# Performance work log

Hardware: AMD Instinct MI355X
Metric: run time of the kernel (lower is better)

The kernel has to match this reference:

```python
import jax, jax.numpy as jnp
import numpy as np

N_NODES = 50000
N_EDGES = 800000
IN_C, HID_C, OUT_C = 128, 128, 64


def setup_inputs() -> dict:
    key = jax.random.key(0)
    k1, k2, k3, k4 = jax.random.split(key, 4)
    x = jax.random.normal(k1, (N_NODES, IN_C), dtype=jnp.float32)
    edge_index = jax.random.randint(k2, (2, N_EDGES), 0, N_NODES, dtype=jnp.int64)
    # Glorot-ish init for weights, zero bias (PyG GCNConv default has bias)
    W1 = jax.random.normal(k3, (IN_C, HID_C), dtype=jnp.float32) * (1.0 / np.sqrt(IN_C))
    b1 = jnp.zeros((HID_C,), dtype=jnp.float32)
    W2 = jax.random.normal(k4, (HID_C, OUT_C), dtype=jnp.float32) * (1.0 / np.sqrt(HID_C))
    b2 = jnp.zeros((OUT_C,), dtype=jnp.float32)
    return {"x": x, "edge_index": edge_index, "W1": W1, "b1": b1, "W2": W2, "b2": b2}


def _gcn_norm(edge_index, num_nodes):
    """PyG gcn_norm: add self-loops, symmetric deg^{-1/2} normalization."""
    loop = jnp.arange(num_nodes, dtype=edge_index.dtype)
    src = jnp.concatenate([edge_index[0], loop])  # [E + N]
    dst = jnp.concatenate([edge_index[1], loop])
    ones = jnp.ones(src.shape[0], dtype=jnp.float32)
    deg = jax.ops.segment_sum(ones, dst, num_segments=num_nodes)  # in-degree incl. self-loop
    dinv = jnp.where(deg > 0, jax.lax.rsqrt(deg), 0.0)
    norm = dinv[src] * dinv[dst]  # [E + N]
    return src, dst, norm


def _gcn_conv(x, W, b, src, dst, norm, num_nodes):
    h = x @ W                                   # [N, C_out] transform first (PyG order)
    msg = h[src] * norm[:, None]                # gather + normalize, [E+N, C_out]
    out = jax.ops.segment_sum(msg, dst, num_segments=num_nodes)  # scatter-add
    return out + b


def reference(x, edge_index, W1, b1, W2, b2):
    N = x.shape[0]
    src, dst, norm = _gcn_norm(edge_index, N)  # graph normalization shared by both layers
    h = jax.nn.relu(_gcn_conv(x, W1, b1, src, dst, norm, N))
    out = _gcn_conv(h, W2, b2, src, dst, norm, N)
    return out
```

## Files before the change

### kernel.cpp

```cpp
#include <hip/hip_runtime.h>
#include <hip/hip_bf16.h>

#define IN_C  128
#define HID_C 128
#define OUT_CC 64
#define BK    128
#define CAPLG 12

using short8  = __attribute__((ext_vector_type(8))) short;
using float4v = __attribute__((ext_vector_type(4))) float;

__device__ __forceinline__ unsigned short f2b(float f) {
    unsigned int u = __float_as_uint(f);
    return (unsigned short)((u + 0x7fffu + ((u >> 16) & 1u)) >> 16);
}
__device__ __forceinline__ unsigned int pack2(float a, float b) {
    return (unsigned int)f2b(a) | ((unsigned int)f2b(b) << 16);
}
__device__ __forceinline__ float2 bf2_to_f2(unsigned int v) {
    float2 r;
    r.x = __uint_as_float(v << 16);
    r.y = __uint_as_float(v & 0xffff0000u);
    return r;
}


__global__ __launch_bounds__(256) void k_setup(const float* __restrict__ W1,
                                               const float* __restrict__ W2,
                                               const int* __restrict__ ei,
                                               unsigned short* __restrict__ w1f,
                                               unsigned short* __restrict__ w2f,
                                               int* __restrict__ flag,
                                               int* __restrict__ bfill, int NBK) {
    int e = blockIdx.x * 256 + threadIdx.x;
    if (e < 16384) {
        int j = e & 7, lane = (e >> 3) & 63, ks = (e >> 9) & 3, nt = e >> 11;
        int k = ks * 32 + ((lane >> 4) << 3) + j;
        int n = nt * 16 + (lane & 15);
        w1f[e] = f2b(W1[k * 128 + n]);
    } else if (e < 16384 + 8192) {
        int e2 = e - 16384;
        int j = e2 & 7, lane = (e2 >> 3) & 63, ks = (e2 >> 9) & 3, nt = e2 >> 11;
        int k = ks * 32 + ((lane >> 4) << 3) + j;
        int n = nt * 16 + (lane & 15);
        w2f[e2] = f2b(W2[k * 64 + n]);
    }
    if (blockIdx.x == 0) {
        for (int i = threadIdx.x; i < NBK; i += 256) bfill[i] = 0;
        if (threadIdx.x == 0) {
            int odd_zero = 1, any_even = 0;
            for (int i = 0; i < 64; ++i) {
                if (ei[2 * i + 1] != 0) odd_zero = 0;
                if (ei[2 * i] != 0) any_even = 1;
            }
            *flag = (odd_zero && any_even) ? 2 : 1;
        }
    }
}

__global__ __launch_bounds__(256) void k_bpart(const int* __restrict__ ei,
                                               const int* __restrict__ flag,
                                               int* __restrict__ bfill,
                                               int* __restrict__ ebuf, int E, int NBK) {
    __shared__ int lh[512];
    __shared__ int lbase[512];
    const int t = threadIdx.x;
    for (int i = t; i < NBK; i += 256) lh[i] = 0;
    __syncthreads();
    const int st = *flag;
    const int base = blockIdx.x * 2048;
    int s[8], d[8];
    #pragma unroll
    for (int j = 0; j < 8; ++j) {
        int i = base + j * 256 + t;
        if (i < E) {
            s[j] = ei[(size_t)st * i];
            d[j] = ei[(size_t)st * ((size_t)E + i)];
            atomicAdd(&lh[d[j] >> 7], 1);
        } else d[j] = -1;
    }
    __syncthreads();
    for (int i = t; i < NBK; i += 256) {
        int c = lh[i];
        lbase[i] = c ? atomicAdd(&bfill[i], c) : 0;
        lh[i] = 0;
    }
    __syncthreads();
    #pragma unroll
    for (int j = 0; j < 8; ++j) {
        if (d[j] >= 0) {
            int b = d[j] >> 7;
            int r = lbase[b] + atomicAdd(&lh[b], 1);
            if (r < (1 << CAPLG))
                ebuf[(b << CAPLG) + r] = s[j] | ((d[j] & (BK - 1)) << 20);
        }
    }
}

__global__ __launch_bounds__(256) void k_blmg1(const int* __restrict__ ebuf,
                                               const int* __restrict__ bfill,
                                               int2* __restrict__ begend,
                                               float* __restrict__ dinv,
                                               int* __restrict__ col,
                                               const float* __restrict__ x,
                                               const unsigned short* __restrict__ w1f,
                                               unsigned short* __restrict__ h,
                                               int N, int NBK) {
    __shared__ unsigned short lds[64 * 136];
    const int t = threadIdx.x;

    if ((int)blockIdx.x < NBK) {
        int* cnt = (int*)lds;
        int* sc  = cnt + BK;
        int* off = sc + BK;
        const int n0 = blockIdx.x * BK;
        const int beg = (int)blockIdx.x << CAPLG;
        const int ecnt = min(bfill[blockIdx.x], 1 << CAPLG);
        if (t < BK) cnt[t] = 0;
        __syncthreads();
        for (int i = t; i < ecnt; i += 256)
            atomicAdd(&cnt[ebuf[beg + i] >> 20], 1);
        __syncthreads();
        if (t < BK) sc[t] = cnt[t];
        __syncthreads();
        for (int o = 1; o < BK; o <<= 1) {
            int v = (t < BK && t >= o) ? sc[t - o] : 0;
            __syncthreads();
            if (t < BK) sc[t] += v;
            __syncthreads();
        }
        if (t < BK) {
            int c = cnt[t];
            off[t] = sc[t] - c;
            if (n0 + t < N) {
                begend[n0 + t] = make_int2(beg + off[t], beg + sc[t]);
                dinv[n0 + t] = rsqrtf((float)c + 1.0f);
            }
            cnt[t] = 0;
        }
        __syncthreads();
        for (int i = t; i < ecnt; i += 256) {
            int e = ebuf[beg + i];
            int dl = e >> 20;
            int p = beg + off[dl] + atomicAdd(&cnt[dl], 1);
            col[p] = e & 0xFFFFF;
        }
        return;
    }

    const int row0 = ((int)blockIdx.x - NBK) * 64;
    {
        int r = t >> 2, cc = (t & 3) * 32;
        int grow = row0 + r;
        unsigned int* dst = (unsigned int*)&lds[r * 136 + cc];
        if (grow < N) {
            const float4* src = (const float4*)(x + (size_t)grow * 128 + cc);
            #pragma unroll
            for (int i = 0; i < 8; ++i) {
                float4 v = src[i];
                dst[2 * i]     = pack2(v.x, v.y);
                dst[2 * i + 1] = pack2(v.z, v.w);
            }
        } else {
            #pragma unroll
            for (int i = 0; i < 16; ++i) dst[i] = 0;
        }
    }
    __syncthreads();
    const int w = t >> 6, lane = t & 63;
    const int quad = lane >> 4, m = lane & 15;
    short8 a[4];
    #pragma unroll
    for (int ks = 0; ks < 4; ++ks)
        a[ks] = *(const short8*)&lds[(w * 16 + m) * 136 + ks * 32 + quad * 8];
    float4v acc[8];
    #pragma unroll
    for (int nt = 0; nt < 8; ++nt) acc[nt] = (float4v){0.f, 0.f, 0.f, 0.f};
    const short8* wf = (const short8*)w1f;
    #pragma unroll
    for (int nt = 0; nt < 8; ++nt)
        #pragma unroll
        for (int ks = 0; ks < 4; ++ks)
            acc[nt] = __builtin_amdgcn_mfma_f32_16x16x32_bf16(a[ks], wf[(nt * 4 + ks) * 64 + lane],
                                                              acc[nt], 0, 0, 0);
    #pragma unroll
    for (int nt = 0; nt < 8; ++nt)
        #pragma unroll
        for (int r = 0; r < 4; ++r) {
            int grow = row0 + w * 16 + quad * 4 + r;
            if (grow < N) h[(size_t)grow * 128 + nt * 16 + m] = f2b(acc[nt][r]);
        }
}

__global__ __launch_bounds__(256) void k_agg128e(const uint4* __restrict__ feat,
                                                 const int2* __restrict__ begend,
                                                 const int* __restrict__ col,
                                                 const float* __restrict__ dinv,
                                                 const float* __restrict__ b1,
                                                 uint4* __restrict__ h1b, int N) {
    const int grp = threadIdx.x >> 4;
    const int l16 = threadIdx.x & 15;
    const int node = blockIdx.x * 16 + grp;
    if (node >= N) return;
    const float dd = dinv[node];
    const int2 be = begend[node];
    const int beg = be.x, end = be.y;
    float a0, a1, a2, a3, a4, a5, a6, a7;
    {
        uint4 sv = feat[(size_t)node * 16 + l16];
        float2 q;
        q = bf2_to_f2(sv.x); a0 = q.x * dd; a1 = q.y * dd;
        q = bf2_to_f2(sv.y); a2 = q.x * dd; a3 = q.y * dd;
        q = bf2_to_f2(sv.z); a4 = q.x * dd; a5 = q.y * dd;
        q = bf2_to_f2(sv.w); a6 = q.x * dd; a7 = q.y * dd;
    }
    int e = beg;
    for (; e + 4 <= end; e += 4) {
        int s0 = col[e], s1 = col[e + 1], s2 = col[e + 2], s3 = col[e + 3];
        float w0 = dinv[s0], w1 = dinv[s1], w2 = dinv[s2], w3 = dinv[s3];
        uint4 u0 = feat[(size_t)s0 * 16 + l16];
        uint4 u1 = feat[(size_t)s1 * 16 + l16];
        uint4 u2 = feat[(size_t)s2 * 16 + l16];
        uint4 u3 = feat[(size_t)s3 * 16 + l16];
        float2 q;
        q = bf2_to_f2(u0.x); a0 += q.x * w0; a1 += q.y * w0;
        q = bf2_to_f2(u0.y); a2 += q.x * w0; a3 += q.y * w0;
        q = bf2_to_f2(u0.z); a4 += q.x * w0; a5 += q.y * w0;
        q = bf2_to_f2(u0.w); a6 += q.x * w0; a7 += q.y * w0;
        q = bf2_to_f2(u1.x); a0 += q.x * w1; a1 += q.y * w1;
        q = bf2_to_f2(u1.y); a2 += q.x * w1; a3 += q.y * w1;
        q = bf2_to_f2(u1.z); a4 += q.x * w1; a5 += q.y * w1;
        q = bf2_to_f2(u1.w); a6 += q.x * w1; a7 += q.y * w1;
        q = bf2_to_f2(u2.x); a0 += q.x * w2; a1 += q.y * w2;
        q = bf2_to_f2(u2.y); a2 += q.x * w2; a3 += q.y * w2;
        q = bf2_to_f2(u2.z); a4 += q.x * w2; a5 += q.y * w2;
        q = bf2_to_f2(u2.w); a6 += q.x * w2; a7 += q.y * w2;
        q = bf2_to_f2(u3.x); a0 += q.x * w3; a1 += q.y * w3;
        q = bf2_to_f2(u3.y); a2 += q.x * w3; a3 += q.y * w3;
        q = bf2_to_f2(u3.z); a4 += q.x * w3; a5 += q.y * w3;
        q = bf2_to_f2(u3.w); a6 += q.x * w3; a7 += q.y * w3;
    }
    for (; e < end; ++e) {
        int s = col[e];
        float w = dinv[s];
        uint4 u = feat[(size_t)s * 16 + l16];
        float2 q;
        q = bf2_to_f2(u.x); a0 += q.x * w; a1 += q.y * w;
        q = bf2_to_f2(u.y); a2 += q.x * w; a3 += q.y * w;
        q = bf2_to_f2(u.z); a4 += q.x * w; a5 += q.y * w;
        q = bf2_to_f2(u.w); a6 += q.x * w; a7 += q.y * w;
    }
    float4 ba = ((const float4*)b1)[2 * l16];
    float4 bb = ((const float4*)b1)[2 * l16 + 1];
    a0 = fmaxf(a0 * dd + ba.x, 0.0f);
    a1 = fmaxf(a1 * dd + ba.y, 0.0f);
    a2 = fmaxf(a2 * dd + ba.z, 0.0f);
    a3 = fmaxf(a3 * dd + ba.w, 0.0f);
    a4 = fmaxf(a4 * dd + bb.x, 0.0f);
    a5 = fmaxf(a5 * dd + bb.y, 0.0f);
    a6 = fmaxf(a6 * dd + bb.z, 0.0f);
    a7 = fmaxf(a7 * dd + bb.w, 0.0f);
    uint4 o;
    o.x = pack2(a0, a1);
    o.y = pack2(a2, a3);
    o.z = pack2(a4, a5);
    o.w = pack2(a6, a7);
    h1b[(size_t)node * 16 + l16] = o;
}

__global__ __launch_bounds__(256) void k_mg2(const unsigned int* __restrict__ h1b,
                                             const unsigned short* __restrict__ w2f,
                                             unsigned short* __restrict__ h2, int N) {
    __shared__ unsigned short lds[64 * 136];
    const int t = threadIdx.x;
    const int row0 = blockIdx.x * 64;
    {
        int r = t >> 2, cc = (t & 3) * 32;
        int grow = row0 + r;
        uint4* dst = (uint4*)&lds[r * 136 + cc];
        if (grow < N) {
            const uint4* src = (const uint4*)(h1b + (size_t)grow * 64 + (cc >> 1));
            #pragma unroll
            for (int i = 0; i < 4; ++i) dst[i] = src[i];
        } else {
            #pragma unroll
            for (int i = 0; i < 4; ++i) dst[i] = (uint4){0, 0, 0, 0};
        }
    }
    __syncthreads();
    const int w = t >> 6, lane = t & 63;
    const int quad = lane >> 4, m = lane & 15;
    short8 a[4];
    #pragma unroll
    for (int ks = 0; ks < 4; ++ks)
        a[ks] = *(const short8*)&lds[(w * 16 + m) * 136 + ks * 32 + quad * 8];
    float4v acc[4];
    #pragma unroll
    for (int nt = 0; nt < 4; ++nt) acc[nt] = (float4v){0.f, 0.f, 0.f, 0.f};
    const short8* wf = (const short8*)w2f;
    #pragma unroll
    for (int nt = 0; nt < 4; ++nt)
        #pragma unroll
        for (int ks = 0; ks < 4; ++ks)
            acc[nt] = __builtin_amdgcn_mfma_f32_16x16x32_bf16(a[ks], wf[(nt * 4 + ks) * 64 + lane],
                                                              acc[nt], 0, 0, 0);
    #pragma unroll
    for (int nt = 0; nt < 4; ++nt)
        #pragma unroll
        for (int r = 0; r < 4; ++r) {
            int grow = row0 + w * 16 + quad * 4 + r;
            if (grow < N) h2[(size_t)grow * 64 + nt * 16 + m] = f2b(acc[nt][r]);
        }
}

__global__ __launch_bounds__(256) void k_agg64(const uint2* __restrict__ feat,
                                               const int2* __restrict__ begend,
                                               const int* __restrict__ col,
                                               const float* __restrict__ dinv,
                                               const float* __restrict__ bias,
                                               float* __restrict__ out, int N) {
    const int grp = threadIdx.x >> 4;
    const int l16 = threadIdx.x & 15;
    const int node = blockIdx.x * 16 + grp;
    if (node >= N) return;
    const float dd = dinv[node];
    const int2 be = begend[node];
    const int beg = be.x, end = be.y;
    float a0, a1, a2, a3;
    {
        uint2 sv = feat[(size_t)node * 16 + l16];
        float2 q;
        q = bf2_to_f2(sv.x); a0 = q.x * dd; a1 = q.y * dd;
        q = bf2_to_f2(sv.y); a2 = q.x * dd; a3 = q.y * dd;
    }
    int e = beg;
    for (; e + 4 <= end; e += 4) {
        int s0 = col[e], s1 = col[e + 1], s2 = col[e + 2], s3 = col[e + 3];
        float w0 = dinv[s0], w1 = dinv[s1], w2 = dinv[s2], w3 = dinv[s3];
        uint2 u0 = feat[(size_t)s0 * 16 + l16];
        uint2 u1 = feat[(size_t)s1 * 16 + l16];
        uint2 u2 = feat[(size_t)s2 * 16 + l16];
        uint2 u3 = feat[(size_t)s3 * 16 + l16];
        float2 q;
        q = bf2_to_f2(u0.x); a0 += q.x * w0; a1 += q.y * w0;
        q = bf2_to_f2(u0.y); a2 += q.x * w0; a3 += q.y * w0;
        q = bf2_to_f2(u1.x); a0 += q.x * w1; a1 += q.y * w1;
        q = bf2_to_f2(u1.y); a2 += q.x * w1; a3 += q.y * w1;
        q = bf2_to_f2(u2.x); a0 += q.x * w2; a1 += q.y * w2;
        q = bf2_to_f2(u2.y); a2 += q.x * w2; a3 += q.y * w2;
        q = bf2_to_f2(u3.x); a0 += q.x * w3; a1 += q.y * w3;
        q = bf2_to_f2(u3.y); a2 += q.x * w3; a3 += q.y * w3;
    }
    for (; e < end; ++e) {
        int s = col[e];
        float w = dinv[s];
        uint2 u = feat[(size_t)s * 16 + l16];
        float2 q;
        q = bf2_to_f2(u.x); a0 += q.x * w; a1 += q.y * w;
        q = bf2_to_f2(u.y); a2 += q.x * w; a3 += q.y * w;
    }
    float4 b = ((const float4*)bias)[l16];
    float4 o;
    o.x = a0 * dd + b.x;
    o.y = a1 * dd + b.y;
    o.z = a2 * dd + b.z;
    o.w = a3 * dd + b.w;
    ((float4*)out)[(size_t)node * 16 + l16] = o;
}

extern "C" void kernel_launch(void* const* d_in, const int* in_sizes, int n_in,
                              void* d_out, int out_size, void* d_ws, size_t ws_size,
                              hipStream_t stream) {
    const float* x  = (const float*)d_in[0];
    const int*   ei = (const int*)d_in[1];
    const float* W1 = (const float*)d_in[2];
    const float* b1 = (const float*)d_in[3];
    const float* W2 = (const float*)d_in[4];
    const float* b2 = (const float*)d_in[5];

    const int N = in_sizes[0] / IN_C;
    const int E = in_sizes[1] / 2;
    const int NBK  = (N + BK - 1) / BK;
    const int NCHK = (E + 2047) / 2048;
    const int NT1  = (N + 63) / 64;

    char* ws = (char*)d_ws;
    int*            flag    = (int*)(ws + 0);
    int*            bfill   = (int*)(ws + 64);
    int2*           begend  = (int2*)(ws + 4096);
    float*          dinv    = (float*)(ws + 404480);
    unsigned short* w1f     = (unsigned short*)(ws + 604672);
    unsigned short* w2f     = (unsigned short*)(ws + 637440);
    int*            ebuf    = (int*)(ws + 655360);
    int*            col     = (int*)(ws + 7061504);
    unsigned short* h       = (unsigned short*)(ws + 13467904);
    uint4*          h1b     = (uint4*)(ws + 26267904);

    k_setup<<<96, 256, 0, stream>>>(W1, W2, ei, w1f, w2f, flag, bfill, NBK);

    k_bpart<<<NCHK, 256, 0, stream>>>(ei, flag, bfill, ebuf, E, NBK);

    k_blmg1<<<NBK + NT1, 256, 0, stream>>>(ebuf, bfill, begend, dinv, col,
                                           x, w1f, h, N, NBK);

    k_agg128e<<<(N + 15) / 16, 256, 0, stream>>>((const uint4*)h, begend, col, dinv, b1, h1b, N);

    unsigned short* h2 = h;
    k_mg2<<<NT1, 256, 0, stream>>>((const unsigned int*)h1b, w2f, h2, N);
    k_agg64<<<(N + 15) / 16, 256, 0, stream>>>((const uint2*)h2, begend, col, dinv, b2, (float*)d_out, N);
}
```

Before: 174.1 us.

## Pre-scale features by source dinv and fuse layer-1 aggregation with second GEMM

Adds a global in-degree count during edge partitioning so the first GEMM can multiply each output row by its own deg^{-1/2} before storing. Because every gathered row is already scaled by its source's normalisation, the aggregation loops no longer do a dinv[s] gather per edge. The layer-1 aggregation kernel now also runs the second MFMA GEMM on its 16-node tile through LDS and pre-scales that result, which removes the h1b round trip and one kernel launch. The cost is one global atomic per edge in the partition kernel and small 16-row GEMM tiles that reload W2 fragments in every block.

```diff
diff --git a/kernel.cpp b/kernel.cpp
--- a/kernel.cpp
+++ b/kernel.cpp
@@ -31,7 +31,8 @@
                                                unsigned short* __restrict__ w1f,
                                                unsigned short* __restrict__ w2f,
                                                int* __restrict__ flag,
-                                               int* __restrict__ bfill, int NBK) {
+                                               int* __restrict__ bfill,
+                                               int* __restrict__ deg, int NBK, int N) {
     int e = blockIdx.x * 256 + threadIdx.x;
     if (e < 16384) {
         int j = e & 7, lane = (e >> 3) & 63, ks = (e >> 9) & 3, nt = e >> 11;
@@ -45,6 +46,7 @@
         int n = nt * 16 + (lane & 15);
         w2f[e2] = f2b(W2[k * 64 + n]);
     }
+    for (int i = e; i < N; i += 96 * 256) deg[i] = 0;
     if (blockIdx.x == 0) {
         for (int i = threadIdx.x; i < NBK; i += 256) bfill[i] = 0;
         if (threadIdx.x == 0) {
@@ -61,6 +63,7 @@
 __global__ __launch_bounds__(256) void k_bpart(const int* __restrict__ ei,
                                                const int* __restrict__ flag,
                                                int* __restrict__ bfill,
+                                               int* __restrict__ deg,
                                                int* __restrict__ ebuf, int E, int NBK) {
     __shared__ int lh[512];
     __shared__ int lbase[512];
@@ -77,6 +80,7 @@
             s[j] = ei[(size_t)st * i];
             d[j] = ei[(size_t)st * ((size_t)E + i)];
             atomicAdd(&lh[d[j] >> 7], 1);
+            atomicAdd(&deg[d[j]], 1);
         } else d[j] = -1;
     }
     __syncthreads();
@@ -104,6 +108,7 @@
                                                int* __restrict__ col,
                                                const float* __restrict__ x,
                                                const unsigned short* __restrict__ w1f,
+                                               const int* __restrict__ deg,
                                                unsigned short* __restrict__ h,
                                                int N, int NBK) {
     __shared__ unsigned short lds[64 * 136];
@@ -183,134 +188,119 @@
         for (int ks = 0; ks < 4; ++ks)
             acc[nt] = __builtin_amdgcn_mfma_f32_16x16x32_bf16(a[ks], wf[(nt * 4 + ks) * 64 + lane],
                                                               acc[nt], 0, 0, 0);
+    float drr[4];
+    #pragma unroll
+    for (int r = 0; r < 4; ++r) {
+        int grow = row0 + w * 16 + quad * 4 + r;
+        drr[r] = (grow < N) ? rsqrtf((float)deg[grow] + 1.0f) : 0.0f;
+    }
     #pragma unroll
     for (int nt = 0; nt < 8; ++nt)
         #pragma unroll
         for (int r = 0; r < 4; ++r) {
             int grow = row0 + w * 16 + quad * 4 + r;
-            if (grow < N) h[(size_t)grow * 128 + nt * 16 + m] = f2b(acc[nt][r]);
-        }
-}
-
-__global__ __launch_bounds__(256) void k_agg128e(const uint4* __restrict__ feat,
-                                                 const int2* __restrict__ begend,
-                                                 const int* __restrict__ col,
-                                                 const float* __restrict__ dinv,
-                                                 const float* __restrict__ b1,
-                                                 uint4* __restrict__ h1b, int N) {
+            if (grow < N) h[(size_t)grow * 128 + nt * 16 + m] = f2b(acc[nt][r] * drr[r]);
+        }
+}
+
+__global__ __launch_bounds__(256) void k_aggmg2(const uint4* __restrict__ feat,
+                                                const int2* __restrict__ begend,
+                                                const int* __restrict__ col,
+                                                const float* __restrict__ dinv,
+                                                const float* __restrict__ b1,
+                                                const unsigned short* __restrict__ w2f,
+                                                unsigned short* __restrict__ h2, int N) {
+    __shared__ unsigned short lds[16 * 136];
+    __shared__ float dvs[16];
     const int grp = threadIdx.x >> 4;
     const int l16 = threadIdx.x & 15;
     const int node = blockIdx.x * 16 + grp;
-    if (node >= N) return;
-    const float dd = dinv[node];
-    const int2 be = begend[node];
-    const int beg = be.x, end = be.y;
-    float a0, a1, a2, a3, a4, a5, a6, a7;
+    float a0 = 0.f, a1 = 0.f, a2 = 0.f, a3 = 0.f, a4 = 0.f, a5 = 0.f, a6 = 0.f, a7 = 0.f;
+    if (node < N) {
+        const float dd = dinv[node];
+        if (l16 == 0) dvs[grp] = dd;
+        const int2 be = begend[node];
+        const int beg = be.x, end = be.y;
+        {
+            uint4 sv = feat[(size_t)node * 16 + l16];
+            float2 q;
+            q = bf2_to_f2(sv.x); a0 = q.x; a1 = q.y;
+            q = bf2_to_f2(sv.y); a2 = q.x; a3 = q.y;
+            q = bf2_to_f2(sv.z); a4 = q.x; a5 = q.y;
+            q = bf2_to_f2(sv.w); a6 = q.x; a7 = q.y;
+        }
+        int e = beg;
+        for (; e + 4 <= end; e += 4) {
+            int s0 = col[e], s1 = col[e + 1], s2 = col[e + 2], s3 = col[e + 3];
+            uint4 u0 = feat[(size_t)s0 * 16 + l16];
+            uint4 u1 = feat[(size_t)s1 * 16 + l16];
+            uint4 u2 = feat[(size_t)s2 * 16 + l16];
+            uint4 u3 = feat[(size_t)s3 * 16 + l16];
+            float2 q;
+            q = bf2_to_f2(u0.x); a0 += q.x; a1 += q.y;
+            q = bf2_to_f2(u0.y); a2 += q.x; a3 += q.y;
+            q = bf2_to_f2(u0.z); a4 += q.x; a5 += q.y;
+            q = bf2_to_f2(u0.w); a6 += q.x; a7 += q.y;
+            q = bf2_to_f2(u1.x); a0 += q.x; a1 += q.y;
+            q = bf2_to_f2(u1.y); a2 += q.x; a3 += q.y;
+            q = bf2_to_f2(u1.z); a4 += q.x; a5 += q.y;
+            q = bf2_to_f2(u1.w); a6 += q.x; a7 += q.y;
+            q = bf2_to_f2(u2.x); a0 += q.x; a1 += q.y;
+            q = bf2_to_f2(u2.y); a2 += q.x; a3 += q.y;
+            q = bf2_to_f2(u2.z); a4 += q.x; a5 += q.y;
+            q = bf2_to_f2(u2.w); a6 += q.x; a7 += q.y;
+            q = bf2_to_f2(u3.x); a0 += q.x; a1 += q.y;
+            q = bf2_to_f2(u3.y); a2 += q.x; a3 += q.y;
+            q = bf2_to_f2(u3.z); a4 += q.x; a5 += q.y;
+            q = bf2_to_f2(u3.w); a6 += q.x; a7 += q.y;
+        }
+        for (; e < end; ++e) {
+            int s = col[e];
+            uint4 u = feat[(size_t)s * 16 + l16];
+            float2 q;
+            q = bf2_to_f2(u.x); a0 += q.x; a1 += q.y;
+            q = bf2_to_f2(u.y); a2 += q.x; a3 += q.y;
+            q = bf2_to_f2(u.z); a4 += q.x; a5 += q.y;
+            q = bf2_to_f2(u.w); a6 += q.x; a7 += q.y;
+        }
+        float4 ba = ((const float4*)b1)[2 * l16];
+        float4 bb = ((const float4*)b1)[2 * l16 + 1];
+        a0 = fmaxf(a0 * dd + ba.x, 0.0f);
+        a1 = fmaxf(a1 * dd + ba.y, 0.0f);
+        a2 = fmaxf(a2 * dd + ba.z, 0.0f);
+        a3 = fmaxf(a3 * dd + ba.w, 0.0f);
+        a4 = fmaxf(a4 * dd + bb.x, 0.0f);
+        a5 = fmaxf(a5 * dd + bb.y, 0.0f);
+        a6 = fmaxf(a6 * dd + bb.z, 0.0f);
+        a7 = fmaxf(a7 * dd + bb.w, 0.0f);
+    } else if (l16 == 0) dvs[grp] = 0.f;
     {
-        uint4 sv = feat[(size_t)node * 16 + l16];
-        float2 q;
-        q = bf2_to_f2(sv.x); a0 = q.x * dd; a1 = q.y * dd;
-        q = bf2_to_f2(sv.y); a2 = q.x * dd; a3 = q.y * dd;
-        q = bf2_to_f2(sv.z); a4 = q.x * dd; a5 = q.y * dd;
-        q = bf2_to_f2(sv.w); a6 = q.x * dd; a7 = q.y * dd;
-    }
-    int e = beg;
-    for (; e + 4 <= end; e += 4) {
-        int s0 = col[e], s1 = col[e + 1], s2 = col[e + 2], s3 = col[e + 3];
-        float w0 = dinv[s0], w1 = dinv[s1], w2 = dinv[s2], w3 = dinv[s3];
-        uint4 u0 = feat[(size_t)s0 * 16 + l16];
-        uint4 u1 = feat[(size_t)s1 * 16 + l16];
-        uint4 u2 = feat[(size_t)s2 * 16 + l16];
-        uint4 u3 = feat[(size_t)s3 * 16 + l16];
-        float2 q;
-        q = bf2_to_f2(u0.x); a0 += q.x * w0; a1 += q.y * w0;
-        q = bf2_to_f2(u0.y); a2 += q.x * w0; a3 += q.y * w0;
-        q = bf2_to_f2(u0.z); a4 += q.x * w0; a5 += q.y * w0;
-        q = bf2_to_f2(u0.w); a6 += q.x * w0; a7 += q.y * w0;
-        q = bf2_to_f2(u1.x); a0 += q.x * w1; a1 += q.y * w1;
-        q = bf2_to_f2(u1.y); a2 += q.x * w1; a3 += q.y * w1;
-        q = bf2_to_f2(u1.z); a4 += q.x * w1; a5 += q.y * w1;
-        q = bf2_to_f2(u1.w); a6 += q.x * w1; a7 += q.y * w1;
-        q = bf2_to_f2(u2.x); a0 += q.x * w2; a1 += q.y * w2;
-        q = bf2_to_f2(u2.y); a2 += q.x * w2; a3 += q.y * w2;
-        q = bf2_to_f2(u2.z); a4 += q.x * w2; a5 += q.y * w2;
-        q = bf2_to_f2(u2.w); a6 += q.x * w2; a7 += q.y * w2;
-        q = bf2_to_f2(u3.x); a0 += q.x * w3; a1 += q.y * w3;
-        q = bf2_to_f2(u3.y); a2 += q.x * w3; a3 += q.y * w3;
-        q = bf2_to_f2(u3.z); a4 += q.x * w3; a5 += q.y * w3;
-        q = bf2_to_f2(u3.w); a6 += q.x * w3; a7 += q.y * w3;
-    }
-    for (; e < end; ++e) {
-        int s = col[e];
-        float w = dinv[s];
-        uint4 u = feat[(size_t)s * 16 + l16];
-        float2 q;
-        q = bf2_to_f2(u.x); a0 += q.x * w; a1 += q.y * w;
-        q = bf2_to_f2(u.y); a2 += q.x * w; a3 += q.y * w;
-        q = bf2_to_f2(u.z); a4 += q.x * w; a5 += q.y * w;
-        q = bf2_to_f2(u.w); a6 += q.x * w; a7 += q.y * w;
-    }
-    float4 ba = ((const float4*)b1)[2 * l16];
-    float4 bb = ((const float4*)b1)[2 * l16 + 1];
-    a0 = fmaxf(a0 * dd + ba.x, 0.0f);
-    a1 = fmaxf(a1 * dd + ba.y, 0.0f);
-    a2 = fmaxf(a2 * dd + ba.z, 0.0f);
-    a3 = fmaxf(a3 * dd + ba.w, 0.0f);
-    a4 = fmaxf(a4 * dd + bb.x, 0.0f);
-    a5 = fmaxf(a5 * dd + bb.y, 0.0f);
-    a6 = fmaxf(a6 * dd + bb.z, 0.0f);
-    a7 = fmaxf(a7 * dd + bb.w, 0.0f);
-    uint4 o;
-    o.x = pack2(a0, a1);
-    o.y = pack2(a2, a3);
-    o.z = pack2(a4, a5);
-    o.w = pack2(a6, a7);
-    h1b[(size_t)node * 16 + l16] = o;
-}
-
-__global__ __launch_bounds__(256) void k_mg2(const unsigned int* __restrict__ h1b,
-                                             const unsigned short* __restrict__ w2f,
-                                             unsigned short* __restrict__ h2, int N) {
-    __shared__ unsigned short lds[64 * 136];
-    const int t = threadIdx.x;
-    const int row0 = blockIdx.x * 64;
-    {
-        int r = t >> 2, cc = (t & 3) * 32;
-        int grow = row0 + r;
-        uint4* dst = (uint4*)&lds[r * 136 + cc];
-        if (grow < N) {
-            const uint4* src = (const uint4*)(h1b + (size_t)grow * 64 + (cc >> 1));
-            #pragma unroll
-            for (int i = 0; i < 4; ++i) dst[i] = src[i];
-        } else {
-            #pragma unroll
-            for (int i = 0; i < 4; ++i) dst[i] = (uint4){0, 0, 0, 0};
-        }
+        uint4 o;
+        o.x = pack2(a0, a1);
+        o.y = pack2(a2, a3);
+        o.z = pack2(a4, a5);
+        o.w = pack2(a6, a7);
+        *(uint4*)&lds[grp * 136 + l16 * 8] = o;
     }
     __syncthreads();
-    const int w = t >> 6, lane = t & 63;
+    const int w = threadIdx.x >> 6, lane = threadIdx.x & 63;
     const int quad = lane >> 4, m = lane & 15;
     short8 a[4];
     #pragma unroll
     for (int ks = 0; ks < 4; ++ks)
-        a[ks] = *(const short8*)&lds[(w * 16 + m) * 136 + ks * 32 + quad * 8];
-    float4v acc[4];
-    #pragma unroll
-    for (int nt = 0; nt < 4; ++nt) acc[nt] = (float4v){0.f, 0.f, 0.f, 0.f};
+        a[ks] = *(const short8*)&lds[m * 136 + ks * 32 + quad * 8];
+    float4v acc = (float4v){0.f, 0.f, 0.f, 0.f};
     const short8* wf = (const short8*)w2f;
     #pragma unroll
-    for (int nt = 0; nt < 4; ++nt)
-        #pragma unroll
-        for (int ks = 0; ks < 4; ++ks)
-            acc[nt] = __builtin_amdgcn_mfma_f32_16x16x32_bf16(a[ks], wf[(nt * 4 + ks) * 64 + lane],
-                                                              acc[nt], 0, 0, 0);
-    #pragma unroll
-    for (int nt = 0; nt < 4; ++nt)
-        #pragma unroll
-        for (int r = 0; r < 4; ++r) {
-            int grow = row0 + w * 16 + quad * 4 + r;
-            if (grow < N) h2[(size_t)grow * 64 + nt * 16 + m] = f2b(acc[nt][r]);
-        }
+    for (int ks = 0; ks < 4; ++ks)
+        acc = __builtin_amdgcn_mfma_f32_16x16x32_bf16(a[ks], wf[(w * 4 + ks) * 64 + lane],
+                                                      acc, 0, 0, 0);
+    const int node0 = blockIdx.x * 16;
+    #pragma unroll
+    for (int r = 0; r < 4; ++r) {
+        int gn = node0 + quad * 4 + r;
+        if (gn < N) h2[(size_t)gn * 64 + w * 16 + m] = f2b(acc[r] * dvs[quad * 4 + r]);
+    }
 }
 
 __global__ __launch_bounds__(256) void k_agg64(const uint2* __restrict__ feat,
@@ -330,34 +320,32 @@
     {
         uint2 sv = feat[(size_t)node * 16 + l16];
         float2 q;
-        q = bf2_to_f2(sv.x); a0 = q.x * dd; a1 = q.y * dd;
-        q = bf2_to_f2(sv.y); a2 = q.x * dd; a3 = q.y * dd;
+        q = bf2_to_f2(sv.x); a0 = q.x; a1 = q.y;
+        q = bf2_to_f2(sv.y); a2 = q.x; a3 = q.y;
     }
     int e = beg;
     for (; e + 4 <= end; e += 4) {
         int s0 = col[e], s1 = col[e + 1], s2 = col[e + 2], s3 = col[e + 3];
-        float w0 = dinv[s0], w1 = dinv[s1], w2 = dinv[s2], w3 = dinv[s3];
         uint2 u0 = feat[(size_t)s0 * 16 + l16];
         uint2 u1 = feat[(size_t)s1 * 16 + l16];
         uint2 u2 = feat[(size_t)s2 * 16 + l16];
         uint2 u3 = feat[(size_t)s3 * 16 + l16];
         float2 q;
-        q = bf2_to_f2(u0.x); a0 += q.x * w0; a1 += q.y * w0;
-        q = bf2_to_f2(u0.y); a2 += q.x * w0; a3 += q.y * w0;
-        q = bf2_to_f2(u1.x); a0 += q.x * w1; a1 += q.y * w1;
-        q = bf2_to_f2(u1.y); a2 += q.x * w1; a3 += q.y * w1;
-        q = bf2_to_f2(u2.x); a0 += q.x * w2; a1 += q.y * w2;
-        q = bf2_to_f2(u2.y); a2 += q.x * w2; a3 += q.y * w2;
-        q = bf2_to_f2(u3.x); a0 += q.x * w3; a1 += q.y * w3;
-        q = bf2_to_f2(u3.y); a2 += q.x * w3; a3 += q.y * w3;
+        q = bf2_to_f2(u0.x); a0 += q.x; a1 += q.y;
+        q = bf2_to_f2(u0.y); a2 += q.x; a3 += q.y;
+        q = bf2_to_f2(u1.x); a0 += q.x; a1 += q.y;
+        q = bf2_to_f2(u1.y); a2 += q.x; a3 += q.y;
+        q = bf2_to_f2(u2.x); a0 += q.x; a1 += q.y;
+        q = bf2_to_f2(u2.y); a2 += q.x; a3 += q.y;
+        q = bf2_to_f2(u3.x); a0 += q.x; a1 += q.y;
+        q = bf2_to_f2(u3.y); a2 += q.x; a3 += q.y;
     }
     for (; e < end; ++e) {
         int s = col[e];
-        float w = dinv[s];
         uint2 u = feat[(size_t)s * 16 + l16];
         float2 q;
-        q = bf2_to_f2(u.x); a0 += q.x * w; a1 += q.y * w;
-        q = bf2_to_f2(u.y); a2 += q.x * w; a3 += q.y * w;
+        q = bf2_to_f2(u.x); a0 += q.x; a1 += q.y;
+        q = bf2_to_f2(u.y); a2 += q.x; a3 += q.y;
     }
     float4 b = ((const float4*)bias)[l16];
     float4 o;
@@ -394,18 +382,19 @@
     int*            ebuf    = (int*)(ws + 655360);
     int*            col     = (int*)(ws + 7061504);
     unsigned short* h       = (unsigned short*)(ws + 13467904);
-    uint4*          h1b     = (uint4*)(ws + 26267904);
-
-    k_setup<<<96, 256, 0, stream>>>(W1, W2, ei, w1f, w2f, flag, bfill, NBK);
-
-    k_bpart<<<NCHK, 256, 0, stream>>>(ei, flag, bfill, ebuf, E, NBK);
+    unsigned short* h2      = (unsigned short*)(ws + 26267904);
+    int*            deg     = (int*)(ws + 32668160);
+
+    k_setup<<<96, 256, 0, stream>>>(W1, W2, ei, w1f, w2f, flag, bfill, deg, NBK, N);
+
+    k_bpart<<<NCHK, 256, 0, stream>>>(ei, flag, bfill, deg, ebuf, E, NBK);
 
     k_blmg1<<<NBK + NT1, 256, 0, stream>>>(ebuf, bfill, begend, dinv, col,
-                                           x, w1f, h, N, NBK);
-
-    k_agg128e<<<(N + 15) / 16, 256, 0, stream>>>((const uint4*)h, begend, col, dinv, b1, h1b, N);
-
-    unsigned short* h2 = h;
-    k_mg2<<<NT1, 256, 0, stream>>>((const unsigned int*)h1b, w2f, h2, N);
-    k_agg64<<<(N + 15) / 16, 256, 0, stream>>>((const uint2*)h2, begend, col, dinv, b2, (float*)d_out, N);
-}
+                                           x, w1f, deg, h, N, NBK);
+
+    k_aggmg2<<<(N + 15) / 16, 256, 0, stream>>>((const uint4*)h, begend, col, dinv, b1,
+                                                w2f, h2, N);
+
+    k_agg64<<<(N + 15) / 16, 256, 0, stream>>>((const uint2*)h2, begend, col, dinv, b2,
+                                               (float*)d_out, N);
+}
```

Result: slower. 195.0 us (+12.0%).
